# Optimization experiments

Hardware: AMD Instinct MI355X
Metric: run time of the kernel (lower is better)

## Reference

```python
import jax, jax.numpy as jnp
import numpy as np

# --- config (Qwen3-Next linear attention defaults) ---
B, S, H = 1, 256, 2048
NK, NV, DK, DV, K = 4, 32, 128, 128, 4
KEY_DIM = NK * DK          # 512
VAL_DIM = NV * DV          # 4096
CONV_DIM = 2 * KEY_DIM + VAL_DIM  # 5120
EPS = 1e-6


def setup_inputs() -> dict:
    key = jax.random.key(0)
    ks = jax.random.split(key, 8)
    rn = lambda k, shape, sc: jax.random.normal(k, shape, jnp.float32) * sc
    return {
        "hidden_states": jax.random.normal(ks[0], (B, S, H), jnp.float32),
        "w_qkvz": rn(ks[1], (2 * KEY_DIM + 2 * VAL_DIM, H), 0.02),  # in_proj_qkvz weight
        "w_ba": rn(ks[2], (2 * NV, H), 0.02),                        # in_proj_ba weight
        "w_out": rn(ks[3], (H, VAL_DIM), 0.02),                      # out_proj weight
        "conv_w": rn(ks[4], (CONV_DIM, 1, K), 0.1),                  # depthwise conv weight [C,1,K]
        "dt_bias": jnp.ones((NV,), jnp.float32),
        "A_log": jnp.zeros((NV,), jnp.float32),
        "norm_w": jnp.ones((DV,), jnp.float32),
    }


def reference(hidden_states, w_qkvz, w_ba, w_out, conv_w, dt_bias, A_log, norm_w):
    b, s, _ = hidden_states.shape
    # input projections (Linear without bias: x @ W.T)
    qkvz = hidden_states @ w_qkvz.T                      # [B,S,9216]
    ba = hidden_states @ w_ba.T                          # [B,S,64]
    q, k, v, z = jnp.split(qkvz, [KEY_DIM, 2 * KEY_DIM, 2 * KEY_DIM + VAL_DIM], axis=-1)
    beta, alpha = jnp.split(ba, 2, axis=-1)              # each [B,S,NV]

    # causal depthwise conv over concat(q,k,v), then silu
    qkv = jnp.concatenate([q, k, v], axis=-1).transpose(0, 2, 1)   # [B,C,S]
    qkv = jax.lax.conv_general_dilated(
        qkv, conv_w, window_strides=(1,), padding=[(K - 1, 0)],
        dimension_numbers=("NCH", "OIH", "NCH"), feature_group_count=CONV_DIM)
    qkv = jax.nn.silu(qkv).transpose(0, 2, 1)            # [B,S,C]
    q, k, v = jnp.split(qkv, [KEY_DIM, 2 * KEY_DIM], axis=-1)

    q = q.reshape(b, s, NK, DK)
    k = k.reshape(b, s, NK, DK)
    v = v.reshape(b, s, NV, DV)
    z = z.reshape(b, s, NV, DV)

    # GQA-style head expansion (repeat_interleave)
    ratio = NV // NK
    q = jnp.repeat(q, ratio, axis=2)                     # [B,S,NV,DK]
    k = jnp.repeat(k, ratio, axis=2)

    # NOTE: original computes g = -softplus(-A_log - alpha) but never uses it (dead code).
    beta_g = jax.nn.sigmoid(beta + dt_bias)[..., None]   # [B,S,NV,1]
    q = q * (DK ** -0.5)

    # naive delta-rule: full outer-product tensor + cumsum (memory-bound)
    kv = jnp.einsum("bsnk,bsnv->bsnkv", k, v * beta_g)   # [B,S,NV,DK,DV]
    out = jnp.einsum("bsnk,bsnkv->bsnv", q, jnp.cumsum(kv, axis=1))  # [B,S,NV,DV]

    # gated RMSNorm over head_v_dim in fp32
    of = out.astype(jnp.float32)
    var = jnp.mean(of * of, axis=-1, keepdims=True)
    of = of * jax.lax.rsqrt(var + EPS) * norm_w
    of = of * jax.nn.silu(z.astype(jnp.float32))

    return of.reshape(b, s, VAL_DIM) @ w_out.T           # [B,S,H]
```

## Files before the change

### kernel.cpp

```cpp
#include <hip/hip_runtime.h>
#include <hip/hip_bf16.h>

#define S_LEN   256
#define HID     2048
#define NVH     32
#define DKD     128
#define DVD     128
#define KEYDIM  512
#define VALDIM  4096
#define CONVDIM 5120
#define QKVZ_N  9216
#define EPS_F   1e-6f

typedef __attribute__((ext_vector_type(8))) short bf16x8;
typedef __attribute__((ext_vector_type(4))) float f32x4;

__device__ __forceinline__ unsigned short f2bf(float f) {
    union { float f; unsigned int i; } v; v.f = f;
    unsigned int x = v.i;
    return (unsigned short)((x + 0x7FFFu + ((x >> 16) & 1u)) >> 16);
}
__device__ __forceinline__ unsigned int pk2(float x, float y) {
    union { __hip_bfloat162 h; unsigned int u; } c;
    c.h = __float22bfloat162_rn(float2{x, y});
    return c.u;
}
__device__ __forceinline__ void gl_lds16(const void* g, void* l) {
    __builtin_amdgcn_global_load_lds(
        (const __attribute__((address_space(1))) unsigned int*)g,
        (__attribute__((address_space(3))) unsigned int*)l,
        16, 0, 0);
}

template<int NT>
__global__ __launch_bounds__(256, 3)
void gemm_db(const unsigned short* __restrict__ A, const float* __restrict__ B,
             float* __restrict__ Cpart, int N, int K, int kc) {
    __shared__ __align__(16) unsigned short As[2][128][64];
    __shared__ __align__(16) unsigned short Bs[2][NT][64];

    const int tid  = threadIdx.x;
    const int lane = tid & 63, wave = tid >> 6;
    const int wm = wave >> 1, wn = wave & 1;
    const int quad = lane >> 4, l16 = lane & 15;
    const int m0 = (blockIdx.x & 1) * 128;
    const int n0 = (blockIdx.x >> 1) * NT;
    const int kbeg = blockIdx.y * kc;
    const int niter = kc >> 6;

    const int a_ro = lane >> 3;
    const int a_gc = (lane & 7) ^ a_ro;

    const int rB = tid >> 2;
    const int cB = (tid & 3) * 16;
    const int swB = rB & 7;

    f32x4 acc[4][2];
#pragma unroll
    for (int i = 0; i < 4; i++)
#pragma unroll
        for (int j = 0; j < 2; j++) acc[i][j] = (f32x4){0.f, 0.f, 0.f, 0.f};

    float4 br[4];
    auto ldB = [&](int kk) {
        const float* p = B + (size_t)(n0 + rB) * K + kk + cB;
        br[0] = *(const float4*)(p);
        br[1] = *(const float4*)(p + 4);
        br[2] = *(const float4*)(p + 8);
        br[3] = *(const float4*)(p + 12);
    };
    auto wrB = [&](int buf) {
        uint4 u0, u1;
        u0.x = pk2(br[0].x, br[0].y); u0.y = pk2(br[0].z, br[0].w);
        u0.z = pk2(br[1].x, br[1].y); u0.w = pk2(br[1].z, br[1].w);
        u1.x = pk2(br[2].x, br[2].y); u1.y = pk2(br[2].z, br[2].w);
        u1.z = pk2(br[3].x, br[3].y); u1.w = pk2(br[3].z, br[3].w);
        int c0 = ((tid & 3) * 2) ^ swB;
        int c1 = ((tid & 3) * 2 + 1) ^ swB;
        *(uint4*)(&Bs[buf][rB][c0 * 8]) = u0;
        *(uint4*)(&Bs[buf][rB][c1 * 8]) = u1;
    };
    auto stageA = [&](int buf, int kk) {
#pragma unroll
        for (int t = 0; t < 4; ++t) {
            int rbase = wave * 32 + t * 8;
            gl_lds16(A + (size_t)(m0 + rbase + a_ro) * K + kk + a_gc * 8,
                     &As[buf][rbase][0]);
        }
    };
    auto compute = [&](int buf) {
#pragma unroll
        for (int ks = 0; ks < 2; ++ks) {
            bf16x8 af[4], bfr[2];
            int c = ((ks * 4 + quad) ^ (l16 & 7)) * 8;
#pragma unroll
            for (int i = 0; i < 4; ++i)
                af[i] = *(const bf16x8*)(&As[buf][wm * 64 + i * 16 + l16][c]);
#pragma unroll
            for (int j = 0; j < 2; ++j)
                bfr[j] = *(const bf16x8*)(&Bs[buf][wn * 32 + j * 16 + l16][c]);
#pragma unroll
            for (int i = 0; i < 4; ++i)
#pragma unroll
                for (int j = 0; j < 2; ++j)
                    acc[i][j] = __builtin_amdgcn_mfma_f32_16x16x32_bf16(af[i], bfr[j], acc[i][j], 0, 0, 0);
        }
    };

    ldB(kbeg);
    stageA(0, kbeg);
    wrB(0);
    if (niter > 1) ldB(kbeg + 64);
    __syncthreads();

    for (int it = 0; it < niter; ++it) {
        if (it + 1 < niter) stageA((it + 1) & 1, kbeg + (it + 1) * 64);
        compute(it & 1);
        if (it + 1 < niter) wrB((it + 1) & 1);
        if (it + 2 < niter) ldB(kbeg + (it + 2) * 64);
        __syncthreads();
    }

    float* C = Cpart + (size_t)blockIdx.y * 256 * N;
#pragma unroll
    for (int i = 0; i < 4; i++)
#pragma unroll
        for (int j = 0; j < 2; j++)
#pragma unroll
            for (int r = 0; r < 4; r++) {
                int row = m0 + wm * 64 + i * 16 + quad * 4 + r;
                int col = n0 + wn * 32 + j * 16 + l16;
                C[(size_t)row * N + col] = acc[i][j][r];
            }
}

template<int P>
__global__ void reduce_sum(const float* __restrict__ part, float* __restrict__ out, int n) {
    int i = (blockIdx.x * 256 + threadIdx.x) * 4;
    if (i >= n) return;
    float4 s = *(const float4*)(part + i);
#pragma unroll
    for (int p = 1; p < P; p++) {
        float4 v = *(const float4*)(part + (size_t)p * n + i);
        s.x += v.x; s.y += v.y; s.z += v.z; s.w += v.w;
    }
    *(float4*)(out + i) = s;
}

__global__ __launch_bounds__(256)
void ba_proj_cvt(const float* __restrict__ hs, const float* __restrict__ w_ba,
                 float* __restrict__ ba, unsigned short* __restrict__ abf) {
    int s = blockIdx.x;
    int n = threadIdx.x & 63, seg = threadIdx.x >> 6;
    const float* x = hs + (size_t)s * HID + seg * 512;
    const float* w = w_ba + (size_t)n * HID + seg * 512;
    float acc = 0.f;
#pragma unroll 4
    for (int k = 0; k < 512; k += 4) {
        float4 xv = *(const float4*)(x + k);
        float4 wv = *(const float4*)(w + k);
        acc += xv.x * wv.x + xv.y * wv.y + xv.z * wv.z + xv.w * wv.w;
    }
    __shared__ float parts[4][64];
    parts[seg][n] = acc;
    {
        int d = threadIdx.x * 8;
        const float4* p = (const float4*)(hs + (size_t)s * HID + d);
        float4 a = p[0], b = p[1];
        uint4 r;
        r.x = pk2(a.x, a.y); r.y = pk2(a.z, a.w);
        r.z = pk2(b.x, b.y); r.w = pk2(b.z, b.w);
        *(uint4*)(abf + (size_t)s * HID + d) = r;
    }
    __syncthreads();
    if (threadIdx.x < 64)
        ba[s * 64 + threadIdx.x] = parts[0][threadIdx.x] + parts[1][threadIdx.x]
                                 + parts[2][threadIdx.x] + parts[3][threadIdx.x];
}

template<int P>
__global__ __launch_bounds__(256)
void sum_conv(const float* __restrict__ part, const float* __restrict__ conv_w,
              float* __restrict__ conv, float* __restrict__ zs) {
    const int s0 = blockIdx.y * 8;
    const int c  = blockIdx.x * 1024 + threadIdx.x * 4;
    auto sum4 = [&](int s) {
        const float* p = part + (size_t)s * QKVZ_N + c;
        float4 v = *(const float4*)p;
#pragma unroll
        for (int q = 1; q < P; q++) {
            float4 w = *(const float4*)(p + (size_t)q * S_LEN * QKVZ_N);
            v.x += w.x; v.y += w.y; v.z += w.z; v.w += w.w;
        }
        return v;
    };
    if (c < CONVDIM) {
        float4 cw[4];
#pragma unroll
        for (int i = 0; i < 4; ++i) cw[i] = *(const float4*)(conv_w + (size_t)(c + i) * 4);
        float4 w0{0,0,0,0}, w1{0,0,0,0}, w2{0,0,0,0};
        for (int s = (s0 >= 3 ? s0 - 3 : 0); s < s0; ++s) { w0 = w1; w1 = w2; w2 = sum4(s); }
        for (int s = s0; s < s0 + 8; ++s) {
            float4 w3 = sum4(s);
            float4 o;
            o.x = w0.x * cw[0].x + w1.x * cw[0].y + w2.x * cw[0].z + w3.x * cw[0].w;
            o.y = w0.y * cw[1].x + w1.y * cw[1].y + w2.y * cw[1].z + w3.y * cw[1].w;
            o.z = w0.z * cw[2].x + w1.z * cw[2].y + w2.z * cw[2].z + w3.z * cw[2].w;
            o.w = w0.w * cw[3].x + w1.w * cw[3].y + w2.w * cw[3].z + w3.w * cw[3].w;
            o.x = o.x / (1.f + __expf(-o.x));
            o.y = o.y / (1.f + __expf(-o.y));
            o.z = o.z / (1.f + __expf(-o.z));
            o.w = o.w / (1.f + __expf(-o.w));
            *(float4*)(conv + (size_t)s * CONVDIM + c) = o;
            w0 = w1; w1 = w2; w2 = w3;
        }
    } else {
        for (int s = s0; s < s0 + 8; ++s) {
            float4 v = sum4(s);
            *(float4*)(zs + (size_t)s * VALDIM + (c - CONVDIM)) = v;
        }
    }
}

__global__ __launch_bounds__(256)
void scores_k(const float* __restrict__ conv, const float* __restrict__ ba,
              const float* __restrict__ dt_bias, float* __restrict__ scores) {
    int p = blockIdx.x;
    int st = (int)((__fsqrt_rn(8.f * p + 1.f) - 1.f) * 0.5f);
    while ((st + 1) * (st + 2) / 2 <= p) st++;
    while (st * (st + 1) / 2 > p) st--;
    int tt = p - st * (st + 1) / 2;
    int hk = blockIdx.y;
    int s0 = st * 16, t0 = tt * 16;
    __shared__ float Qs[16][132], Ks[16][132];
    int tid = threadIdx.x;
    int qoff = hk * DKD;
    int koff = KEYDIM + hk * DKD;
    for (int idx = tid; idx < 16 * 128; idx += 256) {
        int i = idx >> 7, d = idx & 127;
        Qs[i][d] = conv[(size_t)(s0 + i) * CONVDIM + qoff + d];
        Ks[i][d] = conv[(size_t)(t0 + i) * CONVDIM + koff + d];
    }
    __syncthreads();
    int tx = tid & 15, ty = tid >> 4;
    int s = s0 + ty, t = t0 + tx;
    float dot = 0.f;
    for (int d = 0; d < 128; d++) dot += Qs[ty][d] * Ks[tx][d];
    float base = (t <= s) ? dot * 0.08838834764831845f : 0.f;
#pragma unroll
    for (int v = 0; v < 8; v++) {
        int n = hk * 8 + v;
        float b = ba[t * 64 + n] + dt_bias[n];
        float bg = 1.f / (1.f + __expf(-b));
        scores[((size_t)n * 256 + s) * 256 + t] = base * bg;
    }
}

__global__ __launch_bounds__(256)
void attn_rms(const float* __restrict__ scores, const float* __restrict__ conv,
              const float* __restrict__ zs, const float* __restrict__ norm_w,
              unsigned short* __restrict__ normed) {
    int n = blockIdx.y, s0 = blockIdx.x * 16;
    int voff = 2 * KEYDIM + n * DVD;
    __shared__ float Ss[16][17];
    __shared__ float Vs[16][132];
    int tid = threadIdx.x, sy = tid >> 4, dx = tid & 15;
    float acc[8] = {0.f, 0.f, 0.f, 0.f, 0.f, 0.f, 0.f, 0.f};
    for (int t0 = 0; t0 <= s0; t0 += 16) {
        Ss[sy][dx] = scores[((size_t)n * 256 + s0 + sy) * 256 + t0 + dx];
        const float* vp = conv + (size_t)(t0 + sy) * CONVDIM + voff + dx * 8;
        *(float4*)&Vs[sy][dx * 8]     = *(const float4*)vp;
        *(float4*)&Vs[sy][dx * 8 + 4] = *(const float4*)(vp + 4);
        __syncthreads();
#pragma unroll
        for (int j = 0; j < 16; j++) {
            float sv = Ss[sy][j];
#pragma unroll
            for (int r = 0; r < 8; r++) acc[r] += sv * Vs[j][dx + 16 * r];
        }
        __syncthreads();
    }
    float ssq = 0.f;
#pragma unroll
    for (int r = 0; r < 8; r++) ssq += acc[r] * acc[r];
#pragma unroll
    for (int m = 1; m <= 8; m <<= 1) ssq += __shfl_xor(ssq, m, 64);
    float inv = rsqrtf(ssq * (1.f / 128.f) + EPS_F);
    int s = s0 + sy;
#pragma unroll
    for (int r = 0; r < 8; r++) {
        int d = dx + 16 * r;
        float z = zs[(size_t)s * VALDIM + n * DVD + d];
        float sz = z / (1.f + __expf(-z));
        float v = acc[r] * inv * norm_w[d] * sz;
        normed[((size_t)s * NVH + n) * DVD + d] = f2bf(v);
    }
}

extern "C" void kernel_launch(void* const* d_in, const int* in_sizes, int n_in,
                              void* d_out, int out_size, void* d_ws, size_t ws_size,
                              hipStream_t stream) {
    const float* hs      = (const float*)d_in[0];
    const float* w_qkvz  = (const float*)d_in[1];
    const float* w_ba    = (const float*)d_in[2];
    const float* w_out   = (const float*)d_in[3];
    const float* conv_w  = (const float*)d_in[4];
    const float* dt_bias = (const float*)d_in[5];
    const float* norm_w  = (const float*)d_in[7];

    char* ws = (char*)d_ws;
    unsigned short* abf = (unsigned short*)ws; ws += (size_t)S_LEN * HID * 2;
    float* ba   = (float*)ws;  ws += (size_t)S_LEN * 64 * 4;
    float* conv = (float*)ws;  ws += (size_t)S_LEN * CONVDIM * 4;
    float* zs   = (float*)ws;  ws += (size_t)S_LEN * VALDIM * 4;
    char* regB = ws;
    const bool big = ws_size >= (size_t)50 * 1024 * 1024;
    const int sk1 = big ? 4 : 2;
    const int sk2 = big ? 8 : 4;
    float* scratch1 = (float*)regB;
    unsigned short* normed = (unsigned short*)regB;
    float* scratch2 = (float*)(regB + 2097152);
    float* scores   = (float*)(regB + 2097152 + (size_t)sk2 * 2097152);

    ba_proj_cvt<<<S_LEN, 256, 0, stream>>>(hs, w_ba, ba, abf);
    gemm_db<64><<<dim3(2 * (QKVZ_N / 64), sk1), 256, 0, stream>>>(abf, w_qkvz, scratch1, QKVZ_N, HID, HID / sk1);
    if (big) sum_conv<4><<<dim3(9, 32), 256, 0, stream>>>(scratch1, conv_w, conv, zs);
    else     sum_conv<2><<<dim3(9, 32), 256, 0, stream>>>(scratch1, conv_w, conv, zs);
    scores_k<<<dim3(136, 4), 256, 0, stream>>>(conv, ba, dt_bias, scores);
    attn_rms<<<dim3(16, NVH), 256, 0, stream>>>(scores, conv, zs, norm_w, normed);
    gemm_db<64><<<dim3(2 * (HID / 64), sk2), 256, 0, stream>>>(normed, w_out, scratch2, HID, VALDIM, VALDIM / sk2);
    if (big) reduce_sum<8><<<(S_LEN * HID) / 1024, 256, 0, stream>>>(scratch2, (float*)d_out, S_LEN * HID);
    else     reduce_sum<4><<<(S_LEN * HID) / 1024, 256, 0, stream>>>(scratch2, (float*)d_out, S_LEN * HID);
}
```

Measured before the change: 247.0 us.

## Use 512-thread full-M GEMM tiles with single-buffered LDS and deeper split-K

Replaces the double-buffered 128x64-tile GEMM with a 512-thread kernel that covers all 256 rows of M and 128 columns of N per block. Each wave now holds a 4x4 MFMA accumulator. LDS is single-buffered, with explicit syncs between the load and compute phases. The split-K factor doubles for both projections to keep the grid filled, which means more partial buffers to reduce. The goal is more reuse of B per load and fewer redundant weight reads. The cost is less overlap of loads with compute, more register pressure, and extra traffic in the reductions.

```diff
diff --git a/kernel.cpp b/kernel.cpp
--- a/kernel.cpp
+++ b/kernel.cpp
@@ -33,33 +33,31 @@
 }
 
 template<int NT>
-__global__ __launch_bounds__(256, 3)
-void gemm_db(const unsigned short* __restrict__ A, const float* __restrict__ B,
-             float* __restrict__ Cpart, int N, int K, int kc) {
-    __shared__ __align__(16) unsigned short As[2][128][64];
-    __shared__ __align__(16) unsigned short Bs[2][NT][64];
+__global__ __launch_bounds__(512, 4)
+void gemm_w(const unsigned short* __restrict__ A, const float* __restrict__ B,
+            float* __restrict__ Cpart, int N, int K, int kc) {
+    __shared__ __align__(16) unsigned short As[256][64];
+    __shared__ __align__(16) unsigned short Bs[NT][64];
 
     const int tid  = threadIdx.x;
     const int lane = tid & 63, wave = tid >> 6;
-    const int wm = wave >> 1, wn = wave & 1;
+    const int wm = wave & 3, wn = wave >> 2;
     const int quad = lane >> 4, l16 = lane & 15;
-    const int m0 = (blockIdx.x & 1) * 128;
-    const int n0 = (blockIdx.x >> 1) * NT;
+    const int n0 = blockIdx.x * NT;
     const int kbeg = blockIdx.y * kc;
     const int niter = kc >> 6;
 
     const int a_ro = lane >> 3;
     const int a_gc = (lane & 7) ^ a_ro;
-
     const int rB = tid >> 2;
     const int cB = (tid & 3) * 16;
     const int swB = rB & 7;
 
-    f32x4 acc[4][2];
+    f32x4 acc[4][4];
 #pragma unroll
     for (int i = 0; i < 4; i++)
 #pragma unroll
-        for (int j = 0; j < 2; j++) acc[i][j] = (f32x4){0.f, 0.f, 0.f, 0.f};
+        for (int j = 0; j < 4; j++) acc[i][j] = (f32x4){0.f, 0.f, 0.f, 0.f};
 
     float4 br[4];
     auto ldB = [&](int kk) {
@@ -69,7 +67,7 @@
         br[2] = *(const float4*)(p + 8);
         br[3] = *(const float4*)(p + 12);
     };
-    auto wrB = [&](int buf) {
+    auto wrB = [&]() {
         uint4 u0, u1;
         u0.x = pk2(br[0].x, br[0].y); u0.y = pk2(br[0].z, br[0].w);
         u0.z = pk2(br[1].x, br[1].y); u0.w = pk2(br[1].z, br[1].w);
@@ -77,59 +75,58 @@
         u1.z = pk2(br[3].x, br[3].y); u1.w = pk2(br[3].z, br[3].w);
         int c0 = ((tid & 3) * 2) ^ swB;
         int c1 = ((tid & 3) * 2 + 1) ^ swB;
-        *(uint4*)(&Bs[buf][rB][c0 * 8]) = u0;
-        *(uint4*)(&Bs[buf][rB][c1 * 8]) = u1;
-    };
-    auto stageA = [&](int buf, int kk) {
+        *(uint4*)(&Bs[rB][c0 * 8]) = u0;
+        *(uint4*)(&Bs[rB][c1 * 8]) = u1;
+    };
+    auto stageA = [&](int kk) {
 #pragma unroll
         for (int t = 0; t < 4; ++t) {
             int rbase = wave * 32 + t * 8;
-            gl_lds16(A + (size_t)(m0 + rbase + a_ro) * K + kk + a_gc * 8,
-                     &As[buf][rbase][0]);
-        }
-    };
-    auto compute = [&](int buf) {
+            gl_lds16(A + (size_t)(rbase + a_ro) * K + kk + a_gc * 8,
+                     &As[rbase][0]);
+        }
+    };
+    auto compute = [&]() {
 #pragma unroll
         for (int ks = 0; ks < 2; ++ks) {
-            bf16x8 af[4], bfr[2];
+            bf16x8 af[4], bfr[4];
             int c = ((ks * 4 + quad) ^ (l16 & 7)) * 8;
 #pragma unroll
             for (int i = 0; i < 4; ++i)
-                af[i] = *(const bf16x8*)(&As[buf][wm * 64 + i * 16 + l16][c]);
-#pragma unroll
-            for (int j = 0; j < 2; ++j)
-                bfr[j] = *(const bf16x8*)(&Bs[buf][wn * 32 + j * 16 + l16][c]);
+                af[i] = *(const bf16x8*)(&As[wm * 64 + i * 16 + l16][c]);
+#pragma unroll
+            for (int j = 0; j < 4; ++j)
+                bfr[j] = *(const bf16x8*)(&Bs[wn * 64 + j * 16 + l16][c]);
 #pragma unroll
             for (int i = 0; i < 4; ++i)
 #pragma unroll
-                for (int j = 0; j < 2; ++j)
+                for (int j = 0; j < 4; ++j)
                     acc[i][j] = __builtin_amdgcn_mfma_f32_16x16x32_bf16(af[i], bfr[j], acc[i][j], 0, 0, 0);
         }
     };
 
     ldB(kbeg);
-    stageA(0, kbeg);
-    wrB(0);
-    if (niter > 1) ldB(kbeg + 64);
-    __syncthreads();
-
+    stageA(kbeg);
     for (int it = 0; it < niter; ++it) {
-        if (it + 1 < niter) stageA((it + 1) & 1, kbeg + (it + 1) * 64);
-        compute(it & 1);
-        if (it + 1 < niter) wrB((it + 1) & 1);
-        if (it + 2 < niter) ldB(kbeg + (it + 2) * 64);
+        wrB();
         __syncthreads();
+        compute();
+        if (it + 1 < niter) {
+            __syncthreads();
+            ldB(kbeg + (it + 1) * 64);
+            stageA(kbeg + (it + 1) * 64);
+        }
     }
 
     float* C = Cpart + (size_t)blockIdx.y * 256 * N;
 #pragma unroll
     for (int i = 0; i < 4; i++)
 #pragma unroll
-        for (int j = 0; j < 2; j++)
+        for (int j = 0; j < 4; j++)
 #pragma unroll
             for (int r = 0; r < 4; r++) {
-                int row = m0 + wm * 64 + i * 16 + quad * 4 + r;
-                int col = n0 + wn * 32 + j * 16 + l16;
+                int row = wm * 64 + i * 16 + quad * 4 + r;
+                int col = n0 + wn * 64 + j * 16 + l16;
                 C[(size_t)row * N + col] = acc[i][j][r];
             }
 }
@@ -314,21 +311,23 @@
     float* conv = (float*)ws;  ws += (size_t)S_LEN * CONVDIM * 4;
     float* zs   = (float*)ws;  ws += (size_t)S_LEN * VALDIM * 4;
     char* regB = ws;
-    const bool big = ws_size >= (size_t)50 * 1024 * 1024;
-    const int sk1 = big ? 4 : 2;
-    const int sk2 = big ? 8 : 4;
+    const bool big = ws_size >= (size_t)92 * 1024 * 1024;
+    const int sk1 = big ? 8 : 4;
+    const int sk2 = big ? 16 : 8;
     float* scratch1 = (float*)regB;
     unsigned short* normed = (unsigned short*)regB;
     float* scratch2 = (float*)(regB + 2097152);
     float* scores   = (float*)(regB + 2097152 + (size_t)sk2 * 2097152);
 
     ba_proj_cvt<<<S_LEN, 256, 0, stream>>>(hs, w_ba, ba, abf);
-    gemm_db<64><<<dim3(2 * (QKVZ_N / 64), sk1), 256, 0, stream>>>(abf, w_qkvz, scratch1, QKVZ_N, HID, HID / sk1);
-    if (big) sum_conv<4><<<dim3(9, 32), 256, 0, stream>>>(scratch1, conv_w, conv, zs);
-    else     sum_conv<2><<<dim3(9, 32), 256, 0, stream>>>(scratch1, conv_w, conv, zs);
+    if (big) gemm_w<128><<<dim3(QKVZ_N / 128, 8), 512, 0, stream>>>(abf, w_qkvz, scratch1, QKVZ_N, HID, HID / 8);
+    else     gemm_w<128><<<dim3(QKVZ_N / 128, 4), 512, 0, stream>>>(abf, w_qkvz, scratch1, QKVZ_N, HID, HID / 4);
+    if (big) sum_conv<8><<<dim3(9, 32), 256, 0, stream>>>(scratch1, conv_w, conv, zs);
+    else     sum_conv<4><<<dim3(9, 32), 256, 0, stream>>>(scratch1, conv_w, conv, zs);
     scores_k<<<dim3(136, 4), 256, 0, stream>>>(conv, ba, dt_bias, scores);
     attn_rms<<<dim3(16, NVH), 256, 0, stream>>>(scores, conv, zs, norm_w, normed);
-    gemm_db<64><<<dim3(2 * (HID / 64), sk2), 256, 0, stream>>>(normed, w_out, scratch2, HID, VALDIM, VALDIM / sk2);
-    if (big) reduce_sum<8><<<(S_LEN * HID) / 1024, 256, 0, stream>>>(scratch2, (float*)d_out, S_LEN * HID);
-    else     reduce_sum<4><<<(S_LEN * HID) / 1024, 256, 0, stream>>>(scratch2, (float*)d_out, S_LEN * HID);
-}
+    if (big) gemm_w<128><<<dim3(HID / 128, 16), 512, 0, stream>>>(normed, w_out, scratch2, HID, VALDIM, VALDIM / 16);
+    else     gemm_w<128><<<dim3(HID / 128,  8), 512, 0, stream>>>(normed, w_out, scratch2, HID, VALDIM, VALDIM / 8);
+    if (big) reduce_sum<16><<<(S_LEN * HID) / 1024, 256, 0, stream>>>(scratch2, (float*)d_out, S_LEN * HID);
+    else     reduce_sum<8> <<<(S_LEN * HID) / 1024, 256, 0, stream>>>(scratch2, (float*)d_out, S_LEN * HID);
+}
```

Result: slower. 260.2 us (+5.4%).
